# Kernel tuning notes

Hardware: AMD Instinct MI355X
Metric: run time of the kernel (lower is better)

## Reference

```python
import jax, jax.numpy as jnp
import numpy as np

H, DH = 8, 40                      # heads, dim_head
SCALE = DH ** -0.5
NEG = -3.4028235e38                # -finfo(float32).max
EMBDIM, STEPS, EMBEDS = 512, 1000, 50


def _gelu(x):
    return jax.nn.gelu(x, approximate=False)  # torch.nn.GELU default (erf)


def setup_inputs() -> dict:
    key = jax.random.key(0)
    ks = jax.random.split(key, 16)
    b, i, j = 16, 4096, 77
    qd, cd, inner = 320, 768, 320
    s = lambda k, sh, f: jax.random.normal(k, sh, jnp.float32) * f
    bc2 = jnp.tile(jnp.array([0.0, -3.0], jnp.float32), H)  # INITBIAS on class 1
    return dict(
        x=jax.random.normal(ks[0], (b, i, qd), jnp.float32),
        embs=jax.random.normal(ks[1], (b, j, cd), jnp.float32),
        cam=jax.random.uniform(ks[2], (b, i, j), jnp.float32),
        progress=jax.random.uniform(ks[3], (b,), jnp.float32),
        strength=jnp.float32(1.0),
        Wq=s(ks[4], (qd, inner), qd ** -0.5),
        Wk=s(ks[5], (cd, inner), cd ** -0.5),
        Wv=s(ks[6], (cd, inner), cd ** -0.5),
        Wo=s(ks[7], (inner, qd), inner ** -0.5),
        bo=jnp.zeros((qd,), jnp.float32),
        emb1=s(ks[8], (EMBEDS + 1, EMBDIM), 1.0),
        emb2=s(ks[9], (STEPS // EMBEDS, EMBDIM), 1.0),
        Wc1=s(ks[10], (EMBDIM, EMBDIM), EMBDIM ** -0.5),
        bc1=jnp.zeros((EMBDIM,), jnp.float32),
        Wc2=s(ks[11], (EMBDIM, 2 * H), EMBDIM ** -0.5),
        bc2=bc2,
        captiontypes=jax.random.randint(ks[12], (b, j), 0, 5),
    )


def reference(x, embs, cam, progress, strength, Wq, Wk, Wv, Wo, bo,
              emb1, emb2, Wc1, bc1, Wc2, bc2, captiontypes):
    b, i, _ = x.shape
    j = embs.shape[1]
    # projections, split heads: 'b n (h d) -> (b h) n d'
    q = (x @ Wq).reshape(b, i, H, DH).transpose(0, 2, 1, 3).reshape(b * H, i, DH)
    k = (embs @ Wk).reshape(b, j, H, DH).transpose(0, 2, 1, 3).reshape(b * H, j, DH)
    v = (embs @ Wv).reshape(b, j, H, DH).transpose(0, 2, 1, 3).reshape(b * H, j, DH)
    # fp32 QK^T (fp32 already)
    sim = jnp.einsum('bid,bjd->bij', q.astype(jnp.float32), k.astype(jnp.float32))

    # cross_attention_control (CustomCrossAttentionMinimal)
    mask2 = jnp.repeat((captiontypes >= 2)[:, None, :], H, axis=0)  # [(bh),1,j]
    # weight_func under no_grad: std of sim where captiontypes>=2 (unbiased)
    sim_sg = jax.lax.stop_gradient(sim)
    mfull = jnp.broadcast_to(mask2, sim.shape)
    n = mfull.sum().astype(jnp.float32)
    mean = jnp.sum(jnp.where(mfull, sim_sg, 0.0)) / n
    var = jnp.sum(jnp.where(mfull, (sim_sg - mean) ** 2, 0.0)) / (n - 1.0)
    simstd = jnp.sqrt(var)
    wf = jax.lax.stop_gradient(cam * simstd * strength)        # [b,i,j]
    wf = jnp.repeat(wf[:, None], H, axis=1).reshape(b * H, i, j)
    wf = jnp.where(mask2, wf, 0.0)
    useglobal = wf.sum(-1) == 0                                 # [(bh),i]
    wfmax = wf.max(-1, keepdims=True)
    wfb = wf >= (jnp.maximum(wfmax, 0.001) - 0.0001)            # bool [(bh),i,j]
    gmask = jnp.repeat(((captiontypes >= 0) & (captiontypes < 2))[:, None, :], H, axis=0)
    lmask = wfb | (useglobal[:, :, None] & gmask)
    gattn = jax.nn.softmax(jnp.where(gmask, sim, NEG) * SCALE, axis=-1)
    lattn = jax.nn.softmax(jnp.where(lmask, sim, NEG) * SCALE, axis=-1)

    # ProgressClassifier: DiscretizedProgressEmbed -> GELU -> Linear -> GELU -> Linear
    xstep = jnp.minimum(jnp.round(progress * STEPS).astype(jnp.int32), STEPS - 1)
    per = STEPS // EMBEDS  # 20
    e = emb1[xstep // per] + emb2[xstep % per]                  # [b, 512]
    e = _gelu(_gelu(e) @ Wc1 + bc1)
    logits = e @ Wc2 + bc2                                      # [b, 2H]
    pc = jax.nn.softmax(logits.reshape(b, H, 2), axis=-1).reshape(b * H, 2)

    attn = gattn * pc[:, 0, None, None] + lattn * pc[:, 1, None, None]
    out = jnp.einsum('bij,bjd->bid', attn, v.astype(jnp.float32))
    out = out.reshape(b, H, i, DH).transpose(0, 2, 1, 3).reshape(b, i, H * DH)
    return out @ Wo + bo
```

## Files before the change

### kernel.cpp

```cpp
#include <hip/hip_runtime.h>


typedef _Float16 vh8 __attribute__((ext_vector_type(8)));
typedef _Float16 vh4 __attribute__((ext_vector_type(4)));
typedef float    vf4 __attribute__((ext_vector_type(4)));

#define NEGBIG  (-3.4028235e38f)
#define SC2     (0.15811388300841897f * 1.4426950408889634f)
#define INFF    (__builtin_inff())

__device__ __forceinline__ vh8 h8zero() {
  vh8 v;
#pragma unroll
  for (int i = 0; i < 8; ++i) v[i] = (_Float16)0.f;
  return v;
}
__device__ __forceinline__ vf4 f4zero() {
  vf4 v;
#pragma unroll
  for (int i = 0; i < 4; ++i) v[i] = 0.f;
  return v;
}
__device__ __forceinline__ float gelu_exact(float x) {
  return 0.5f * x * (1.0f + erff(x * 0.70710678118654752f));
}
__device__ __forceinline__ unsigned swzA(int row) {
  return (unsigned)(((row & 7) << 4) ^ (((row >> 3) & 1) << 5));
}
__device__ __forceinline__ unsigned swzB(int row) {
  return (unsigned)((row & 7) << 4);
}
__device__ __forceinline__ void glds16(const void* g, void* l) {
  __builtin_amdgcn_global_load_lds((const __attribute__((address_space(1))) unsigned*)g,
                                   (__attribute__((address_space(3))) unsigned*)l, 16, 0, 0);
}

__global__ __launch_bounds__(256) void transpose_kernel(
    const float* __restrict__ Wq, const float* __restrict__ Wk,
    const float* __restrict__ Wv, const float* __restrict__ Wo,
    _Float16* __restrict__ WqT, _Float16* __restrict__ WkvT, _Float16* __restrict__ WoT)
{
  __shared__ float ts[32][33];
  int tile = blockIdx.x;
  const float* src; _Float16* dst; int dstK, rowOff;
  if (tile < 100)      { src = Wq; dst = WqT;  dstK = 320; rowOff = 0; }
  else if (tile < 340) { src = Wk; dst = WkvT; dstK = 768; rowOff = 0;   tile -= 100; }
  else if (tile < 580) { src = Wv; dst = WkvT; dstK = 768; rowOff = 320; tile -= 340; }
  else                 { src = Wo; dst = WoT;  dstK = 320; rowOff = 0;   tile -= 580; }
  int kb = tile / 10, nb = tile - kb * 10;
  int k0 = kb * 32, n0 = nb * 32;
  int r = threadIdx.x >> 5, c = threadIdx.x & 31;
#pragma unroll
  for (int p = 0; p < 4; ++p)
    ts[r + p * 8][c] = src[(size_t)(k0 + r + p * 8) * 320 + n0 + c];
  __syncthreads();
#pragma unroll
  for (int p = 0; p < 4; ++p)
    dst[(size_t)(rowOff + n0 + r + p * 8) * dstK + k0 + c] = (_Float16)ts[c][r + p * 8];
}

__global__ __launch_bounds__(256) void vtrans_kernel(
    const _Float16* __restrict__ vf, unsigned* __restrict__ vTg32)
{
  const int b = blockIdx.x, h = blockIdx.y, t = threadIdx.x;
  unsigned* out = vTg32 + (size_t)(b * 8 + h) * 3072;
#pragma unroll
  for (int p = 0; p < 12; ++p) {
    int idx = t + p * 256;
    int d = idx >> 6;
    int u = idx & 63;
    int c = u >> 2, pr = u & 3;
    int sd = (int)(swzA(d) >> 4);
    int j0 = ((c ^ sd) << 3) + pr * 2;
    unsigned lo = 0, hi = 0;
    if (d < 40) {
      if (j0 < 77)     lo = *(const unsigned short*)(vf + (size_t)(b * 77 + j0) * 640 + h * 40 + d);
      if (j0 + 1 < 77) hi = *(const unsigned short*)(vf + (size_t)(b * 77 + j0 + 1) * 640 + h * 40 + d);
    }
    out[idx] = lo | (hi << 16);
  }
}

__global__ __launch_bounds__(256) void kv_gemm_kernel(
    const float* __restrict__ Ap, const _Float16* __restrict__ Bt,
    _Float16* __restrict__ Cp, int M, int N, int K)
{
  __shared__ _Float16 As[128 * 64];
  __shared__ _Float16 Bs[160 * 64];
  const int t = threadIdx.x, lane = t & 63, wave = t >> 6;
  const int m0 = blockIdx.x * 128;
  const int n0 = blockIdx.y * 160;
  const int l15 = lane & 15, l4 = lane >> 4;
  const int wbase = t & ~63;

  vf4 acc[2][10];
#pragma unroll
  for (int a = 0; a < 2; ++a)
#pragma unroll
    for (int bq = 0; bq < 10; ++bq) acc[a][bq] = f4zero();

  for (int k0 = 0; k0 < K; k0 += 64) {
    __syncthreads();
#pragma unroll
    for (int p = 0; p < 8; ++p) {
      int idx = t + p * 256;
      int row = idx >> 4, g4 = idx & 15;
      int m = m0 + row;
      vh4 hw;
      hw[0] = (_Float16)0.f; hw[1] = (_Float16)0.f; hw[2] = (_Float16)0.f; hw[3] = (_Float16)0.f;
      if (m < M) {
        const float* ap = Ap + (size_t)m * K + k0 + g4 * 4;
        float4 f = *(const float4*)ap;
        hw[0] = (_Float16)f.x; hw[1] = (_Float16)f.y; hw[2] = (_Float16)f.z; hw[3] = (_Float16)f.w;
      }
      unsigned byte = (unsigned)(row * 128 + g4 * 8) ^ swzB(row);
      *(vh4*)((char*)As + byte) = hw;
    }
#pragma unroll
    for (int p = 0; p < 5; ++p) {
      int idx = t + p * 256;
      int n = idx >> 3, c8 = idx & 7;
      const _Float16* src = Bt + (size_t)(n0 + n) * K + k0 + ((c8 ^ (n & 7)) << 3);
      glds16(src, (char*)Bs + (size_t)(p * 256 + wbase) * 16);
    }
    __syncthreads();
#pragma unroll
    for (int ks = 0; ks < 2; ++ks) {
      vh8 av[2];
#pragma unroll
      for (int mt = 0; mt < 2; ++mt) {
        int row = wave * 32 + mt * 16 + l15;
        unsigned byte = (unsigned)(row * 128 + (ks * 32 + l4 * 8) * 2) ^ swzB(row);
        av[mt] = *(const vh8*)((const char*)As + byte);
      }
#pragma unroll
      for (int nt = 0; nt < 10; ++nt) {
        int n = nt * 16 + l15;
        unsigned byte = (unsigned)(n * 128 + (ks * 32 + l4 * 8) * 2) ^ swzB(n);
        vh8 bv = *(const vh8*)((const char*)Bs + byte);
        acc[0][nt] = __builtin_amdgcn_mfma_f32_16x16x32_f16(av[0], bv, acc[0][nt], 0, 0, 0);
        acc[1][nt] = __builtin_amdgcn_mfma_f32_16x16x32_f16(av[1], bv, acc[1][nt], 0, 0, 0);
      }
    }
  }
#pragma unroll
  for (int mt = 0; mt < 2; ++mt)
#pragma unroll
    for (int nt = 0; nt < 10; ++nt) {
      int n = n0 + nt * 16 + l15;
#pragma unroll
      for (int r = 0; r < 4; ++r) {
        int m = m0 + wave * 32 + mt * 16 + l4 * 4 + r;
        if (m < M) Cp[(size_t)m * N + n] = (_Float16)acc[mt][nt][r];
      }
    }
}

__global__ __launch_bounds__(256) void qproj_kernel(
    const float* __restrict__ x, const _Float16* __restrict__ Bt,
    _Float16* __restrict__ qhm)
{
  __shared__ __align__(16) char smem[40960];
  _Float16* Bs = (_Float16*)smem;
  const int t = threadIdx.x, lane = t & 63, wave = t >> 6;
  const int m0 = blockIdx.x * 64;
  const int l15 = lane & 15, l4 = lane >> 4;
  const int wbase = t & ~63;
  const int rg = wave >> 1, cg = wave & 1;

  vf4 acc[2][10];
#pragma unroll
  for (int a = 0; a < 2; ++a)
#pragma unroll
    for (int bq = 0; bq < 10; ++bq) acc[a][bq] = f4zero();

  for (int kc = 0; kc < 5; ++kc) {
    int k0 = kc * 64;
    __syncthreads();
#pragma unroll
    for (int p = 0; p < 10; ++p) {
      int idx = t + p * 256;
      int n = idx >> 3, c8 = idx & 7;
      glds16(Bt + (size_t)n * 320 + k0 + ((c8 ^ (n & 7)) << 3),
             (char*)Bs + (size_t)(p * 256 + wbase) * 16);
    }
    __syncthreads();
#pragma unroll
    for (int ks = 0; ks < 2; ++ks) {
      int k = k0 + ks * 32 + l4 * 8;
      vh8 av[2];
#pragma unroll
      for (int mt = 0; mt < 2; ++mt) {
        int row = m0 + rg * 32 + mt * 16 + l15;
        const float* ap = x + (size_t)row * 320 + k;
        float4 f0 = *(const float4*)ap;
        float4 f1 = *(const float4*)(ap + 4);
        vh8 hv;
        hv[0] = (_Float16)f0.x; hv[1] = (_Float16)f0.y; hv[2] = (_Float16)f0.z; hv[3] = (_Float16)f0.w;
        hv[4] = (_Float16)f1.x; hv[5] = (_Float16)f1.y; hv[6] = (_Float16)f1.z; hv[7] = (_Float16)f1.w;
        av[mt] = hv;
      }
#pragma unroll
      for (int nt = 0; nt < 10; ++nt) {
        int n = cg * 160 + nt * 16 + l15;
        unsigned byte = (unsigned)(n * 128 + (ks * 32 + l4 * 8) * 2) ^ swzB(n);
        vh8 bv = *(const vh8*)((const char*)Bs + byte);
        acc[0][nt] = __builtin_amdgcn_mfma_f32_16x16x32_f16(av[0], bv, acc[0][nt], 0, 0, 0);
        acc[1][nt] = __builtin_amdgcn_mfma_f32_16x16x32_f16(av[1], bv, acc[1][nt], 0, 0, 0);
      }
    }
  }

  __syncthreads();
#pragma unroll
  for (int mt = 0; mt < 2; ++mt)
#pragma unroll
    for (int nt = 0; nt < 10; ++nt) {
      int col = cg * 160 + nt * 16 + l15;
#pragma unroll
      for (int r = 0; r < 4; ++r) {
        int lr = rg * 32 + mt * 16 + l4 * 4 + r;
        unsigned byte = (unsigned)(lr * 640 + col * 2) ^ swzB(lr);
        *(_Float16*)(smem + byte) = (_Float16)acc[mt][nt][r];
      }
    }
  __syncthreads();
#pragma unroll
  for (int p = 0; p < 10; ++p) {
    int idx = t + p * 256;
    int h = idx / 320;
    int rem = idx - h * 320;
    int lrow = rem / 5;
    int c = rem - lrow * 5;
    unsigned sb = (unsigned)(lrow * 640 + h * 80 + c * 16) ^ swzB(lrow);
    vh8 v = *(const vh8*)(smem + sb);
    int gi = m0 + lrow;
    int bb = gi >> 12, ii = gi & 4095;
    *(vh8*)(qhm + ((size_t)(bb * 8 + h) * 4096 + ii) * 40 + c * 8) = v;
  }
}

__global__ __launch_bounds__(256) void oproj_kernel(
    const _Float16* __restrict__ hohm, const _Float16* __restrict__ Bt,
    const float* __restrict__ bias, float* __restrict__ out)
{
  __shared__ __align__(16) _Float16 Bs[320 * 64];
  const int t = threadIdx.x, lane = t & 63, wave = t >> 6;
  const int m0 = blockIdx.x * 64;
  const int l15 = lane & 15, l4 = lane >> 4;
  const int wbase = t & ~63;
  const int rg = wave >> 1, cg = wave & 1;

  vf4 acc[2][10];
#pragma unroll
  for (int a = 0; a < 2; ++a)
#pragma unroll
    for (int bq = 0; bq < 10; ++bq) acc[a][bq] = f4zero();

  for (int kc = 0; kc < 5; ++kc) {
    int k0 = kc * 64;
    __syncthreads();
#pragma unroll
    for (int p = 0; p < 10; ++p) {
      int idx = t + p * 256;
      int n = idx >> 3, c8 = idx & 7;
      glds16(Bt + (size_t)n * 320 + k0 + ((c8 ^ (n & 7)) << 3),
             (char*)Bs + (size_t)(p * 256 + wbase) * 16);
    }
    __syncthreads();
#pragma unroll
    for (int ks = 0; ks < 2; ++ks) {
      int k = k0 + ks * 32 + l4 * 8;
      int hh = k / 40, d = k - hh * 40;
      vh8 av[2];
#pragma unroll
      for (int mt = 0; mt < 2; ++mt) {
        int gi = m0 + rg * 32 + mt * 16 + l15;
        int bb = gi >> 12, ii = gi & 4095;
        av[mt] = *(const vh8*)(hohm + ((size_t)(bb * 8 + hh) * 4096 + ii) * 40 + d);
      }
#pragma unroll
      for (int nt = 0; nt < 10; ++nt) {
        int n = cg * 160 + nt * 16 + l15;
        unsigned byte = (unsigned)(n * 128 + (ks * 32 + l4 * 8) * 2) ^ swzB(n);
        vh8 bv = *(const vh8*)((const char*)Bs + byte);
        acc[0][nt] = __builtin_amdgcn_mfma_f32_16x16x32_f16(av[0], bv, acc[0][nt], 0, 0, 0);
        acc[1][nt] = __builtin_amdgcn_mfma_f32_16x16x32_f16(av[1], bv, acc[1][nt], 0, 0, 0);
      }
    }
  }
#pragma unroll
  for (int mt = 0; mt < 2; ++mt)
#pragma unroll
    for (int nt = 0; nt < 10; ++nt) {
      int n = cg * 160 + nt * 16 + l15;
      float bias_v = bias[n];
#pragma unroll
      for (int r = 0; r < 4; ++r) {
        int m = m0 + rg * 32 + mt * 16 + l4 * 4 + r;
        out[(size_t)m * 320 + n] = acc[mt][nt][r] + bias_v;
      }
    }
}

__global__ __launch_bounds__(256) void classifier_kernel(
    const float* __restrict__ progress,
    const float* __restrict__ emb1, const float* __restrict__ emb2,
    const float* __restrict__ Wc1, const float* __restrict__ bc1,
    const float* __restrict__ Wc2, const float* __restrict__ bc2,
    float* __restrict__ pcb)
{
  __shared__ float g[512];
  __shared__ float h1[512];
  __shared__ float lg[16];
  const int b = blockIdx.x;
  const int t = threadIdx.x;

  float pr = progress[b];
  int xstep = (int)rintf(pr * 1000.0f);
  if (xstep > 999) xstep = 999;
  int a = xstep / 20;
  int r = xstep - a * 20;

  for (int d = t; d < 512; d += 256) {
    float e = emb1[a * 512 + d] + emb2[r * 512 + d];
    g[d] = gelu_exact(e);
  }
  __syncthreads();
  for (int n = t; n < 512; n += 256) {
    float acc = bc1[n];
    for (int d = 0; d < 512; ++d) acc = fmaf(g[d], Wc1[d * 512 + n], acc);
    h1[n] = gelu_exact(acc);
  }
  __syncthreads();
  if (t < 16) {
    float acc = bc2[t];
    for (int d = 0; d < 512; ++d) acc = fmaf(h1[d], Wc2[d * 16 + t], acc);
    lg[t] = acc;
  }
  __syncthreads();
  if (t < 8) {
    float a0 = lg[2 * t], a1 = lg[2 * t + 1];
    float mx = fmaxf(a0, a1);
    float e0 = __expf(a0 - mx), e1 = __expf(a1 - mx);
    float inv = 1.0f / (e0 + e1);
    pcb[(b * 8 + t) * 2 + 0] = e0 * inv;
    pcb[(b * 8 + t) * 2 + 1] = e1 * inv;
  }
}

__global__ __launch_bounds__(256) void std_kernel(
    const _Float16* __restrict__ qhm, const _Float16* __restrict__ kf,
    const int* __restrict__ ctypes, double* __restrict__ partials)
{
  __shared__ __align__(16) _Float16 qt[64 * 40];
  const int t = threadIdx.x, lane = t & 63, wave = t >> 6;
  const int it = blockIdx.x, b = blockIdx.y, h = blockIdx.z;
  const int i0 = it * 64;
  const int l15 = lane & 15, l4 = lane >> 4;

  const _Float16* qsrc = qhm + ((size_t)(b * 8 + h) * 4096 + i0) * 40;
  glds16(qsrc + t * 8, (char*)qt + t * 16);
  if (t < 64) glds16(qsrc + (256 + t) * 8, (char*)qt + (256 + t) * 16);
  __syncthreads();

  int qrow = wave * 16 + l15;
  vh8 a0 = *(const vh8*)((const char*)qt + qrow * 80 + l4 * 16);
  vh8 a1 = h8zero();
  if (l4 == 0) a1 = *(const vh8*)((const char*)qt + qrow * 80 + 64);

  double S = 0.0, S2 = 0.0;
#pragma unroll
  for (int jt = 0; jt < 5; ++jt) {
    int j = jt * 16 + l15;
    bool valid = (j < 77);
    vh8 b0 = h8zero(), b1 = h8zero();
    int ctj = -1;
    if (valid) {
      const _Float16* kp = kf + (size_t)(b * 77 + j) * 640 + h * 40;
      b0 = *(const vh8*)(kp + l4 * 8);
      if (l4 == 0) b1 = *(const vh8*)(kp + 32);
      ctj = ctypes[b * 77 + j];
    }
    vf4 s = f4zero();
    s = __builtin_amdgcn_mfma_f32_16x16x32_f16(a0, b0, s, 0, 0, 0);
    s = __builtin_amdgcn_mfma_f32_16x16x32_f16(a1, b1, s, 0, 0, 0);
    if (ctj >= 2) {
#pragma unroll
      for (int r = 0; r < 4; ++r) {
        double sv = (double)s[r];
        S += sv; S2 += sv * sv;
      }
    }
  }
#pragma unroll
  for (int off = 32; off > 0; off >>= 1) {
    S += __shfl_xor(S, off);
    S2 += __shfl_xor(S2, off);
  }
  if (lane == 0) {
    int idx = (((b * 64 + it) * 8) + h) * 4 + wave;
    partials[2 * idx + 0] = S;
    partials[2 * idx + 1] = S2;
  }
}

__global__ __launch_bounds__(256) void finalize_kernel(
    const double* __restrict__ partials, const int* __restrict__ ctypes,
    float* __restrict__ ssb)
{
  __shared__ double rs[256];
  __shared__ double rs2[256];
  __shared__ int rc[256];
  const int t = threadIdx.x;
  double S = 0.0, S2 = 0.0;
#pragma unroll
  for (int p = 0; p < 128; ++p) {
    int idx = t + p * 256;
    S += partials[2 * idx + 0];
    S2 += partials[2 * idx + 1];
  }
  int c = 0;
#pragma unroll
  for (int p = 0; p < 5; ++p) {
    int idx = t + p * 256;
    if (idx < 1232) c += (ctypes[idx] >= 2) ? 1 : 0;
  }
  rs[t] = S; rs2[t] = S2; rc[t] = c;
  __syncthreads();
  for (int off = 128; off > 0; off >>= 1) {
    if (t < off) { rs[t] += rs[t + off]; rs2[t] += rs2[t + off]; rc[t] += rc[t + off]; }
    __syncthreads();
  }
  if (t == 0) {
    double n = (double)rc[0] * 8.0 * 4096.0;
    double mean = rs[0] / n;
    double var = (rs2[0] - n * mean * mean) / (n - 1.0);
    ssb[0] = (float)sqrt(var > 0.0 ? var : 0.0);
  }
}

__global__ __launch_bounds__(256) void lmask_kernel(
    const float* __restrict__ cam, const int* __restrict__ ctypes,
    const float* __restrict__ ssb, const float* __restrict__ strengthp,
    unsigned* __restrict__ lmp)
{
  __shared__ float camt[64 * 81];
  __shared__ unsigned char gmv[96];
  __shared__ unsigned char m2v[96];
  const int t = threadIdx.x;
  const int it = blockIdx.x, b = blockIdx.y;
  const int i0 = it * 64;

  if (t < 96) {
    int j = t;
    int ct = (j < 77) ? ctypes[b * 77 + j] : -1;
    gmv[j] = (j < 77 && ct >= 0 && ct < 2) ? 1 : 0;
    m2v[j] = (j < 77 && ct >= 2) ? 1 : 0;
  }
#pragma unroll
  for (int p = 0; p < 20; ++p) {
    int idx = t + p * 256;
    int row = idx / 80;
    int j = idx - row * 80;
    camt[row * 81 + j] = (j < 77) ? cam[((size_t)b * 4096 + i0 + row) * 77 + j] : 0.f;
  }
  __syncthreads();

  const float ss = ssb[0];
  const float st = strengthp[0];
  int row = t >> 2, qd = t & 3;
  float wfv[20];
  float wmax = 0.f, wsum = 0.f;
#pragma unroll
  for (int m = 0; m < 20; ++m) {
    int j = qd + 4 * m;
    float wf = 0.f;
    if (j < 77 && m2v[j]) wf = (camt[row * 81 + j] * ss) * st;
    wfv[m] = wf;
    wmax = fmaxf(wmax, wf);
    wsum += wf;
  }
  wmax = fmaxf(wmax, __shfl_xor(wmax, 1));
  wmax = fmaxf(wmax, __shfl_xor(wmax, 2));
  wsum += __shfl_xor(wsum, 1);
  wsum += __shfl_xor(wsum, 2);
  float thr = fmaxf(wmax, 0.001f) - 0.0001f;
  bool ug = (wsum == 0.f);
  unsigned wbits = 0u;
#pragma unroll
  for (int m = 0; m < 20; ++m) {
    int j = qd + 4 * m;
    bool lv = (wfv[m] >= thr) || (ug && (j < 77) && gmv[j]);
    if (lv) wbits |= (1u << m);
  }
  lmp[((size_t)b * 4096 + i0 + row) * 4 + qd] = wbits;
}

__global__ __launch_bounds__(256) void attn_kernel(
    const _Float16* __restrict__ qhm, const _Float16* __restrict__ kf,
    const unsigned* __restrict__ vTg32, const int* __restrict__ ctypes,
    const float* __restrict__ pcb, const unsigned* __restrict__ lmp,
    _Float16* __restrict__ hohm)
{
  __shared__ _Float16 vT[48 * 128];
  __shared__ _Float16 attnbuf[64 * 128];
  __shared__ __align__(16) _Float16 qt[64 * 40];
  __shared__ unsigned lmw[256];
  __shared__ float gbf[96];
  __shared__ float nbf[96];

  const int t = threadIdx.x, lane = t & 63, wave = t >> 6;
  const int it = blockIdx.x, b = blockIdx.y, h = blockIdx.z;
  const int i0 = it * 64;
  const int l15 = lane & 15, l4 = lane >> 4;

  if (t < 96) {
    int j = t;
    bool valid = (j < 77);
    int ct = valid ? ctypes[b * 77 + j] : -1;
    bool gm = valid && ct >= 0 && ct < 2;
    gbf[j] = gm ? 0.f : (valid ? NEGBIG : -INFF);
    nbf[j] = valid ? NEGBIG : -INFF;
  }
  lmw[t] = lmp[((size_t)b * 4096 + i0) * 4 + t];

  const _Float16* qsrc = qhm + ((size_t)(b * 8 + h) * 4096 + i0) * 40;
  glds16(qsrc + t * 8, (char*)qt + t * 16);
  if (t < 64) glds16(qsrc + (256 + t) * 8, (char*)qt + (256 + t) * 16);

  {
    const unsigned* src0 = vTg32 + (size_t)(b * 8 + h) * 3072;
#pragma unroll
    for (int p = 0; p < 3; ++p) {
      int idx = t + p * 256;
      glds16(src0 + idx * 4, (char*)vT + (size_t)(p * 256 + (t & ~63)) * 16);
    }
  }
#pragma unroll
  for (int p = 0; p < 2; ++p) {
    int idx = t + p * 256;
    int row = idx >> 3, c = idx & 7;
    unsigned byte = (unsigned)(row * 256 + 160 + c * 4) ^ swzA(row);
    *(unsigned*)((char*)attnbuf + byte) = 0u;
  }

  vh8 k0v[5], k1v[5];
#pragma unroll
  for (int jt = 0; jt < 5; ++jt) {
    int j = jt * 16 + l15;
    k0v[jt] = h8zero(); k1v[jt] = h8zero();
    if (j < 77) {
      const _Float16* kp = kf + (size_t)(b * 77 + j) * 640 + h * 40;
      k0v[jt] = *(const vh8*)(kp + l4 * 8);
      if (l4 == 0) k1v[jt] = *(const vh8*)(kp + 32);
    }
  }

  __syncthreads();

  const int myrow = wave * 16 + l15;
  vh8 qf0 = *(const vh8*)((const char*)qt + myrow * 80 + l4 * 16);
  vh8 qf1 = h8zero();
  if (l4 == 0) qf1 = *(const vh8*)((const char*)qt + myrow * 80 + 64);

  vf4 sacc[5];
#pragma unroll
  for (int jt = 0; jt < 5; ++jt) sacc[jt] = f4zero();
#pragma unroll
  for (int jt = 0; jt < 5; ++jt) {
    sacc[jt] = __builtin_amdgcn_mfma_f32_16x16x32_f16(k0v[jt], qf0, sacc[jt], 0, 0, 0);
    sacc[jt] = __builtin_amdgcn_mfma_f32_16x16x32_f16(k1v[jt], qf1, sacc[jt], 0, 0, 0);
  }

  const float pc0 = pcb[(b * 8 + h) * 2 + 0];
  const float pc1 = pcb[(b * 8 + h) * 2 + 1];
  unsigned wbits[4];
#pragma unroll
  for (int r = 0; r < 4; ++r) wbits[r] = lmw[myrow * 4 + r];

  float gv[5][4], lv[5][4];
  float mg = -INFF, ml = -INFF;
#pragma unroll
  for (int jt = 0; jt < 5; ++jt) {
    int jbase = jt * 16 + l4 * 4;
    float4 gb4 = *(const float4*)&gbf[jbase];
    float4 nb4 = *(const float4*)&nbf[jbase];
    const float* gbp = (const float*)&gb4;
    const float* nbp = (const float*)&nb4;
#pragma unroll
    for (int r = 0; r < 4; ++r) {
      float sv = sacc[jt][r];
      float g = fmaf(sv, SC2, gbp[r]);
      unsigned bit = (wbits[r] >> (jt * 4 + l4)) & 1u;
      float l = fmaf(sv, SC2, bit ? 0.f : nbp[r]);
      gv[jt][r] = g; lv[jt][r] = l;
      mg = fmaxf(mg, g); ml = fmaxf(ml, l);
    }
  }
  mg = fmaxf(mg, __shfl_xor(mg, 16)); mg = fmaxf(mg, __shfl_xor(mg, 32));
  ml = fmaxf(ml, __shfl_xor(ml, 16)); ml = fmaxf(ml, __shfl_xor(ml, 32));
  float sG = 0.f, sL = 0.f;
#pragma unroll
  for (int jt = 0; jt < 5; ++jt)
#pragma unroll
    for (int r = 0; r < 4; ++r) {
      float eg = exp2f(gv[jt][r] - mg);
      float el = exp2f(lv[jt][r] - ml);
      gv[jt][r] = eg; lv[jt][r] = el;
      sG += eg; sL += el;
    }
  sG += __shfl_xor(sG, 16); sG += __shfl_xor(sG, 32);
  sL += __shfl_xor(sL, 16); sL += __shfl_xor(sL, 32);
  float rG = pc0 / sG, rL = pc1 / sL;
  {
    unsigned swz = swzA(myrow);
    unsigned rowbase = (unsigned)(myrow * 256);
#pragma unroll
    for (int jt = 0; jt < 5; ++jt) {
      vh4 w;
#pragma unroll
      for (int r = 0; r < 4; ++r)
        w[r] = (_Float16)fmaf(gv[jt][r], rG, lv[jt][r] * rL);
      unsigned byte = (rowbase + (unsigned)((jt * 16 + l4 * 4) * 2)) ^ swz;
      *(vh4*)((char*)attnbuf + byte) = w;
    }
  }
  __syncthreads();

  vf4 oacc[3];
#pragma unroll
  for (int nt = 0; nt < 3; ++nt) oacc[nt] = f4zero();
#pragma unroll
  for (int ks = 0; ks < 3; ++ks) {
    int arow = wave * 16 + l15;
    unsigned abyte = (unsigned)(arow * 256 + (ks * 32 + l4 * 8) * 2) ^ swzA(arow);
    vh8 pa = *(const vh8*)((const char*)attnbuf + abyte);
#pragma unroll
    for (int nt = 0; nt < 3; ++nt) {
      int n = nt * 16 + l15;
      unsigned byte = (unsigned)(n * 256 + (ks * 32 + l4 * 8) * 2) ^ swzA(n);
      vh8 vb = *(const vh8*)((const char*)vT + byte);
      oacc[nt] = __builtin_amdgcn_mfma_f32_16x16x32_f16(pa, vb, oacc[nt], 0, 0, 0);
    }
  }
#pragma unroll
  for (int nt = 0; nt < 3; ++nt) {
    int d = nt * 16 + l15;
    if (d < 40) {
#pragma unroll
      for (int r = 0; r < 4; ++r) {
        int m = wave * 16 + l4 * 4 + r;
        qt[m * 40 + d] = (_Float16)oacc[nt][r];
      }
    }
  }
  __syncthreads();

  _Float16* obase = hohm + ((size_t)(b * 8 + h) * 4096 + i0) * 40;
  {
    vh8 v = *(const vh8*)((const char*)qt + t * 16);
    *(vh8*)(obase + t * 8) = v;
  }
  if (t < 64) {
    vh8 v = *(const vh8*)((const char*)qt + (256 + t) * 16);
    *(vh8*)(obase + (256 + t) * 8) = v;
  }
}

extern "C" void kernel_launch(void* const* d_in, const int* in_sizes, int n_in,
                              void* d_out, int out_size, void* d_ws, size_t ws_size,
                              hipStream_t stream)
{
  const float* x        = (const float*)d_in[0];
  const float* embs     = (const float*)d_in[1];
  const float* cam      = (const float*)d_in[2];
  const float* progress = (const float*)d_in[3];
  const float* strength = (const float*)d_in[4];
  const float* Wq       = (const float*)d_in[5];
  const float* Wk       = (const float*)d_in[6];
  const float* Wv       = (const float*)d_in[7];
  const float* Wo       = (const float*)d_in[8];
  const float* bo       = (const float*)d_in[9];
  const float* emb1     = (const float*)d_in[10];
  const float* emb2     = (const float*)d_in[11];
  const float* Wc1      = (const float*)d_in[12];
  const float* bc1      = (const float*)d_in[13];
  const float* Wc2      = (const float*)d_in[14];
  const float* bc2      = (const float*)d_in[15];
  const int*   ctypes   = (const int*)d_in[16];

  char* w = (char*)d_ws;
  auto alloc = [&](size_t bytes) { char* p = w; w += (bytes + 255) & ~(size_t)255; return p; };
  _Float16* qhm   = (_Float16*)alloc(65536ull * 320 * 2);
  _Float16* hohm  = (_Float16*)alloc(65536ull * 320 * 2);
  _Float16* kvb   = (_Float16*)alloc(1232ull * 640 * 2);
  unsigned* vTg   = (unsigned*)alloc(128ull * 3072 * 4);
  _Float16* WqT   = (_Float16*)alloc(320ull * 320 * 2);
  _Float16* WkvT  = (_Float16*)alloc(640ull * 768 * 2);
  _Float16* WoT   = (_Float16*)alloc(320ull * 320 * 2);
  unsigned* lmp   = (unsigned*)alloc(65536ull * 4 * 4);
  float*    pcb   = (float*)alloc(256 * 4);
  double*   part  = (double*)alloc(32768ull * 2 * 8);
  float*    ssb   = (float*)alloc(256);

  transpose_kernel<<<680, 256, 0, stream>>>(Wq, Wk, Wv, Wo, WqT, WkvT, WoT);
  classifier_kernel<<<16, 256, 0, stream>>>(progress, emb1, emb2, Wc1, bc1, Wc2, bc2, pcb);
  kv_gemm_kernel<<<dim3(10, 4), 256, 0, stream>>>(embs, WkvT, kvb, 1232, 640, 768);
  vtrans_kernel<<<dim3(16, 8), 256, 0, stream>>>(kvb + 320, vTg);
  qproj_kernel<<<1024, 256, 0, stream>>>(x, WqT, qhm);
  std_kernel<<<dim3(64, 16, 8), 256, 0, stream>>>(qhm, kvb, ctypes, part);
  finalize_kernel<<<1, 256, 0, stream>>>(part, ctypes, ssb);
  lmask_kernel<<<dim3(64, 16), 256, 0, stream>>>(cam, ctypes, ssb, strength, lmp);
  attn_kernel<<<dim3(64, 16, 8), 256, 0, stream>>>(qhm, kvb, vTg, ctypes, pcb, lmp, hohm);
  oproj_kernel<<<1024, 256, 0, stream>>>(hohm, WoT, bo, (float*)d_out);
}
```

Measured before the change: 300.7 us.

## Prefetch A operands into registers in qproj/oproj and simplify kv GEMM

The qproj and oproj kernels now double-buffer their A-operand global loads in registers, issuing the next K-chunk's loads before the barrier so their latency overlaps the MFMA work on the current chunk. The kv GEMM drops shared-memory staging entirely, reads A and B straight from global memory with smaller 64-row tiles, and launches twice as many blocks for better parallelism on a small problem. The cost is higher register pressure in the projection kernels and uncoalesced, non-reused B loads in the kv GEMM. An unused lambda is also left behind.

```diff
diff --git a/kernel.cpp b/kernel.cpp
--- a/kernel.cpp
+++ b/kernel.cpp
@@ -83,75 +83,55 @@
 
 __global__ __launch_bounds__(256) void kv_gemm_kernel(
     const float* __restrict__ Ap, const _Float16* __restrict__ Bt,
-    _Float16* __restrict__ Cp, int M, int N, int K)
-{
-  __shared__ _Float16 As[128 * 64];
-  __shared__ _Float16 Bs[160 * 64];
+    _Float16* __restrict__ Cp)
+{
   const int t = threadIdx.x, lane = t & 63, wave = t >> 6;
-  const int m0 = blockIdx.x * 128;
+  const int m0 = blockIdx.x * 64;
   const int n0 = blockIdx.y * 160;
   const int l15 = lane & 15, l4 = lane >> 4;
-  const int wbase = t & ~63;
-
-  vf4 acc[2][10];
+  const int rg = wave >> 1, cg = wave & 1;
+
+  vf4 acc[2][5];
 #pragma unroll
   for (int a = 0; a < 2; ++a)
 #pragma unroll
-    for (int bq = 0; bq < 10; ++bq) acc[a][bq] = f4zero();
-
-  for (int k0 = 0; k0 < K; k0 += 64) {
-    __syncthreads();
-#pragma unroll
-    for (int p = 0; p < 8; ++p) {
-      int idx = t + p * 256;
-      int row = idx >> 4, g4 = idx & 15;
-      int m = m0 + row;
-      vh4 hw;
-      hw[0] = (_Float16)0.f; hw[1] = (_Float16)0.f; hw[2] = (_Float16)0.f; hw[3] = (_Float16)0.f;
-      if (m < M) {
-        const float* ap = Ap + (size_t)m * K + k0 + g4 * 4;
-        float4 f = *(const float4*)ap;
-        hw[0] = (_Float16)f.x; hw[1] = (_Float16)f.y; hw[2] = (_Float16)f.z; hw[3] = (_Float16)f.w;
-      }
-      unsigned byte = (unsigned)(row * 128 + g4 * 8) ^ swzB(row);
-      *(vh4*)((char*)As + byte) = hw;
-    }
-#pragma unroll
-    for (int p = 0; p < 5; ++p) {
-      int idx = t + p * 256;
-      int n = idx >> 3, c8 = idx & 7;
-      const _Float16* src = Bt + (size_t)(n0 + n) * K + k0 + ((c8 ^ (n & 7)) << 3);
-      glds16(src, (char*)Bs + (size_t)(p * 256 + wbase) * 16);
-    }
-    __syncthreads();
-#pragma unroll
-    for (int ks = 0; ks < 2; ++ks) {
-      vh8 av[2];
-#pragma unroll
-      for (int mt = 0; mt < 2; ++mt) {
-        int row = wave * 32 + mt * 16 + l15;
-        unsigned byte = (unsigned)(row * 128 + (ks * 32 + l4 * 8) * 2) ^ swzB(row);
-        av[mt] = *(const vh8*)((const char*)As + byte);
-      }
-#pragma unroll
-      for (int nt = 0; nt < 10; ++nt) {
-        int n = nt * 16 + l15;
-        unsigned byte = (unsigned)(n * 128 + (ks * 32 + l4 * 8) * 2) ^ swzB(n);
-        vh8 bv = *(const vh8*)((const char*)Bs + byte);
-        acc[0][nt] = __builtin_amdgcn_mfma_f32_16x16x32_f16(av[0], bv, acc[0][nt], 0, 0, 0);
-        acc[1][nt] = __builtin_amdgcn_mfma_f32_16x16x32_f16(av[1], bv, acc[1][nt], 0, 0, 0);
-      }
+    for (int bq = 0; bq < 5; ++bq) acc[a][bq] = f4zero();
+
+#pragma unroll 2
+  for (int kk = 0; kk < 24; ++kk) {
+    int k = kk * 32 + l4 * 8;
+    vh8 av[2];
+#pragma unroll
+    for (int mt = 0; mt < 2; ++mt) {
+      int row = m0 + rg * 32 + mt * 16 + l15;
+      av[mt] = h8zero();
+      if (row < 1232) {
+        const float* ap = Ap + (size_t)row * 768 + k;
+        float4 f0 = *(const float4*)ap;
+        float4 f1 = *(const float4*)(ap + 4);
+        vh8 hv;
+        hv[0] = (_Float16)f0.x; hv[1] = (_Float16)f0.y; hv[2] = (_Float16)f0.z; hv[3] = (_Float16)f0.w;
+        hv[4] = (_Float16)f1.x; hv[5] = (_Float16)f1.y; hv[6] = (_Float16)f1.z; hv[7] = (_Float16)f1.w;
+        av[mt] = hv;
+      }
+    }
+#pragma unroll
+    for (int nt = 0; nt < 5; ++nt) {
+      int n = n0 + cg * 80 + nt * 16 + l15;
+      vh8 bv = *(const vh8*)(Bt + (size_t)n * 768 + k);
+      acc[0][nt] = __builtin_amdgcn_mfma_f32_16x16x32_f16(av[0], bv, acc[0][nt], 0, 0, 0);
+      acc[1][nt] = __builtin_amdgcn_mfma_f32_16x16x32_f16(av[1], bv, acc[1][nt], 0, 0, 0);
     }
   }
 #pragma unroll
   for (int mt = 0; mt < 2; ++mt)
 #pragma unroll
-    for (int nt = 0; nt < 10; ++nt) {
-      int n = n0 + nt * 16 + l15;
+    for (int nt = 0; nt < 5; ++nt) {
+      int n = n0 + cg * 80 + nt * 16 + l15;
 #pragma unroll
       for (int r = 0; r < 4; ++r) {
-        int m = m0 + wave * 32 + mt * 16 + l4 * 4 + r;
-        if (m < M) Cp[(size_t)m * N + n] = (_Float16)acc[mt][nt][r];
+        int m = m0 + rg * 32 + mt * 16 + l4 * 4 + r;
+        if (m < 1232) Cp[(size_t)m * 640 + n] = (_Float16)acc[mt][nt][r];
       }
     }
 }
@@ -167,6 +147,8 @@
   const int l15 = lane & 15, l4 = lane >> 4;
   const int wbase = t & ~63;
   const int rg = wave >> 1, cg = wave & 1;
+  const float* arow0 = x + (size_t)(m0 + rg * 32 + l15) * 320 + l4 * 8;
+  const float* arow1 = x + (size_t)(m0 + rg * 32 + 16 + l15) * 320 + l4 * 8;
 
   vf4 acc[2][10];
 #pragma unroll
@@ -174,6 +156,16 @@
 #pragma unroll
     for (int bq = 0; bq < 10; ++bq) acc[a][bq] = f4zero();
 
+  float4 fA[8], fB[8];
+#pragma unroll
+  for (int ks = 0; ks < 2; ++ks) {
+    fA[ks * 4 + 0] = *(const float4*)(arow0 + ks * 32);
+    fA[ks * 4 + 1] = *(const float4*)(arow0 + ks * 32 + 4);
+    fA[ks * 4 + 2] = *(const float4*)(arow1 + ks * 32);
+    fA[ks * 4 + 3] = *(const float4*)(arow1 + ks * 32 + 4);
+  }
+
+#pragma unroll
   for (int kc = 0; kc < 5; ++kc) {
     int k0 = kc * 64;
     __syncthreads();
@@ -184,17 +176,26 @@
       glds16(Bt + (size_t)n * 320 + k0 + ((c8 ^ (n & 7)) << 3),
              (char*)Bs + (size_t)(p * 256 + wbase) * 16);
     }
+    float4* nxt = (kc & 1) ? fA : fB;
+    if (kc < 4) {
+      int k0n = k0 + 64;
+#pragma unroll
+      for (int ks = 0; ks < 2; ++ks) {
+        nxt[ks * 4 + 0] = *(const float4*)(arow0 + k0n + ks * 32);
+        nxt[ks * 4 + 1] = *(const float4*)(arow0 + k0n + ks * 32 + 4);
+        nxt[ks * 4 + 2] = *(const float4*)(arow1 + k0n + ks * 32);
+        nxt[ks * 4 + 3] = *(const float4*)(arow1 + k0n + ks * 32 + 4);
+      }
+    }
     __syncthreads();
+    float4* cur = (kc & 1) ? fB : fA;
 #pragma unroll
     for (int ks = 0; ks < 2; ++ks) {
-      int k = k0 + ks * 32 + l4 * 8;
       vh8 av[2];
 #pragma unroll
       for (int mt = 0; mt < 2; ++mt) {
-        int row = m0 + rg * 32 + mt * 16 + l15;
-        const float* ap = x + (size_t)row * 320 + k;
-        float4 f0 = *(const float4*)ap;
-        float4 f1 = *(const float4*)(ap + 4);
+        float4 f0 = cur[ks * 4 + mt * 2 + 0];
+        float4 f1 = cur[ks * 4 + mt * 2 + 1];
         vh8 hv;
         hv[0] = (_Float16)f0.x; hv[1] = (_Float16)f0.y; hv[2] = (_Float16)f0.z; hv[3] = (_Float16)f0.w;
         hv[4] = (_Float16)f1.x; hv[5] = (_Float16)f1.y; hv[6] = (_Float16)f1.z; hv[7] = (_Float16)f1.w;
@@ -251,12 +252,29 @@
   const int wbase = t & ~63;
   const int rg = wave >> 1, cg = wave & 1;
 
+  const int gi0 = m0 + rg * 32 + l15;
+  const int gi1 = gi0 + 16;
+  const int bb0 = gi0 >> 12, ii0 = gi0 & 4095;
+  const int bb1 = gi1 >> 12, ii1 = gi1 & 4095;
+
   vf4 acc[2][10];
 #pragma unroll
   for (int a = 0; a < 2; ++a)
 #pragma unroll
     for (int bq = 0; bq < 10; ++bq) acc[a][bq] = f4zero();
 
+  auto aload = [&](int k) -> vh8 { return h8zero(); };
+
+  vh8 hA[4], hB[4];
+#pragma unroll
+  for (int ks = 0; ks < 2; ++ks) {
+    int k = ks * 32 + l4 * 8;
+    int hh = k / 40, d = k - hh * 40;
+    hA[ks * 2 + 0] = *(const vh8*)(hohm + ((size_t)(bb0 * 8 + hh) * 4096 + ii0) * 40 + d);
+    hA[ks * 2 + 1] = *(const vh8*)(hohm + ((size_t)(bb1 * 8 + hh) * 4096 + ii1) * 40 + d);
+  }
+
+#pragma unroll
   for (int kc = 0; kc < 5; ++kc) {
     int k0 = kc * 64;
     __syncthreads();
@@ -267,25 +285,27 @@
       glds16(Bt + (size_t)n * 320 + k0 + ((c8 ^ (n & 7)) << 3),
              (char*)Bs + (size_t)(p * 256 + wbase) * 16);
     }
+    vh8* nxt = (kc & 1) ? hA : hB;
+    if (kc < 4) {
+#pragma unroll
+      for (int ks = 0; ks < 2; ++ks) {
+        int k = k0 + 64 + ks * 32 + l4 * 8;
+        int hh = k / 40, d = k - hh * 40;
+        nxt[ks * 2 + 0] = *(const vh8*)(hohm + ((size_t)(bb0 * 8 + hh) * 4096 + ii0) * 40 + d);
+        nxt[ks * 2 + 1] = *(const vh8*)(hohm + ((size_t)(bb1 * 8 + hh) * 4096 + ii1) * 40 + d);
+      }
+    }
     __syncthreads();
+    vh8* cur = (kc & 1) ? hB : hA;
 #pragma unroll
     for (int ks = 0; ks < 2; ++ks) {
-      int k = k0 + ks * 32 + l4 * 8;
-      int hh = k / 40, d = k - hh * 40;
-      vh8 av[2];
-#pragma unroll
-      for (int mt = 0; mt < 2; ++mt) {
-        int gi = m0 + rg * 32 + mt * 16 + l15;
-        int bb = gi >> 12, ii = gi & 4095;
-        av[mt] = *(const vh8*)(hohm + ((size_t)(bb * 8 + hh) * 4096 + ii) * 40 + d);
-      }
 #pragma unroll
       for (int nt = 0; nt < 10; ++nt) {
         int n = cg * 160 + nt * 16 + l15;
         unsigned byte = (unsigned)(n * 128 + (ks * 32 + l4 * 8) * 2) ^ swzB(n);
         vh8 bv = *(const vh8*)((const char*)Bs + byte);
-        acc[0][nt] = __builtin_amdgcn_mfma_f32_16x16x32_f16(av[0], bv, acc[0][nt], 0, 0, 0);
-        acc[1][nt] = __builtin_amdgcn_mfma_f32_16x16x32_f16(av[1], bv, acc[1][nt], 0, 0, 0);
+        acc[0][nt] = __builtin_amdgcn_mfma_f32_16x16x32_f16(cur[ks * 2 + 0], bv, acc[0][nt], 0, 0, 0);
+        acc[1][nt] = __builtin_amdgcn_mfma_f32_16x16x32_f16(cur[ks * 2 + 1], bv, acc[1][nt], 0, 0, 0);
       }
     }
   }
@@ -706,7 +726,7 @@
 
   transpose_kernel<<<680, 256, 0, stream>>>(Wq, Wk, Wv, Wo, WqT, WkvT, WoT);
   classifier_kernel<<<16, 256, 0, stream>>>(progress, emb1, emb2, Wc1, bc1, Wc2, bc2, pcb);
-  kv_gemm_kernel<<<dim3(10, 4), 256, 0, stream>>>(embs, WkvT, kvb, 1232, 640, 768);
+  kv_gemm_kernel<<<dim3(20, 4), 256, 0, stream>>>(embs, WkvT, kvb);
   vtrans_kernel<<<dim3(16, 8), 256, 0, stream>>>(kvb + 320, vTg);
   qproj_kernel<<<1024, 256, 0, stream>>>(x, WqT, qhm);
   std_kernel<<<dim3(64, 16, 8), 256, 0, stream>>>(qhm, kvb, ctypes, part);
```

Result: faster. 283.2 us (-5.8%).
